# Optimization experiments

Measured on AMD Instinct MI355X. Metric: run time of the kernel, lower is better.

## Reference

```python
import jax, jax.numpy as jnp
import numpy as np

TEMPERATURE = 0.07
TAU_THRESHOLD = 0.5

B, D, K = 32768, 512, 2048


def _l2_normalize(x, axis=-1, eps=1e-12):
    # matches torch F.normalize: x / max(||x||, eps)
    n = jnp.linalg.norm(x, axis=axis, keepdims=True)
    return x / jnp.maximum(n, eps)


def setup_inputs() -> dict:
    key = jax.random.key(0)
    k1, k2, k3, k4 = jax.random.split(key, 4)
    embeddings = jax.random.normal(k1, (B, D), dtype=jnp.float32)
    best_similarity = jax.random.uniform(k2, (B,), dtype=jnp.float32)
    global_prototypes = jax.random.normal(k3, (K, D), dtype=jnp.float32)
    prototype_confidence = jax.random.uniform(k4, (K,), dtype=jnp.float32)
    return {
        "embeddings": embeddings,
        "best_similarity": best_similarity,
        "global_prototypes": global_prototypes,
        "prototype_confidence": prototype_confidence,
    }


def reference(embeddings, best_similarity, global_prototypes, prototype_confidence):
    en = _l2_normalize(embeddings, axis=1)          # [B, D]
    pn = _l2_normalize(global_prototypes, axis=1)   # [K, D]
    sims = jnp.einsum("bd,kd->bk", en, pn)          # [B, K] cosine sims
    best_proto_idx = jnp.argmax(sims, axis=1)       # [B]

    logits = sims / TEMPERATURE
    log_probs = jax.nn.log_softmax(logits, axis=1)  # [B, K]
    probs = jnp.exp(log_probs)
    entropy = -jnp.sum(probs * log_probs, axis=1)   # [B]
    max_entropy = jnp.log(jnp.float32(K))
    entropy_norm = entropy / (max_entropy + 1e-8)
    tau_adaptive = TAU_THRESHOLD - 0.2 * entropy_norm

    # confidence_weighted gating
    batch_conf = prototype_confidence[best_proto_idx]                     # [B]
    sigmoid_gate = jax.nn.sigmoid((best_similarity - tau_adaptive) / TEMPERATURE)
    gate = batch_conf * sigmoid_gate                                      # [B]

    target_protos = pn[best_proto_idx]                                    # [B, D]
    dist = jnp.linalg.norm(en - target_protos, axis=1)                    # [B]
    L_proto = jnp.mean(gate * dist)
    return (L_proto, gate)
```

## Files before the change

### kernel.cpp

```cpp
#include <hip/hip_runtime.h>
#include <math.h>


#define NB 32768
#define ND 512
#define NK 2048
#define TEMPR 0.07f
#define INV_T 14.285714285714286f
#define DX 1.4285714e-4f

typedef unsigned short u16;
typedef unsigned long long u64;
using bf16x8 = __attribute__((ext_vector_type(8))) short;
using u16x8 = __attribute__((ext_vector_type(8))) unsigned short;
using f32x16 = __attribute__((ext_vector_type(16))) float;

__device__ inline u16 bf_hi(float x) {
  unsigned u = __float_as_uint(x);
  u = u + 0x7FFFu + ((u >> 16) & 1u);
  return (u16)(u >> 16);
}
__device__ inline float bf_tof(u16 h) {
  return __uint_as_float(((unsigned)h) << 16);
}
__device__ inline void gload_lds16(const void* g, void* l) {
  __builtin_amdgcn_global_load_lds((const __attribute__((address_space(1))) void*)g,
                                   (__attribute__((address_space(3))) void*)l, 16, 0, 0);
}
#define MF(a, b, c) __builtin_amdgcn_mfma_f32_32x32x16_bf16((a), (b), (c), 0, 0, 0)

#define WAIT_LGKM0 { asm volatile("s_waitcnt lgkmcnt(0)" ::: "memory"); \
                     __builtin_amdgcn_sched_barrier(0); }
#define WAIT_VM10  { asm volatile("s_waitcnt vmcnt(10)" ::: "memory"); \
                     __builtin_amdgcn_sched_barrier(0); }
#define SBAR       { __builtin_amdgcn_s_barrier(); \
                     __builtin_amdgcn_sched_barrier(0); }

__global__ __launch_bounds__(256) void kprep_p(const float* __restrict__ P,
                                               u16* __restrict__ Phi,
                                               u16* __restrict__ Plo,
                                               float* __restrict__ invp,
                                               int* __restrict__ cnt) {
  if (blockIdx.x == 0 && threadIdx.x == 0) *cnt = 0;
  const int lane = threadIdx.x & 63, w = threadIdx.x >> 6;
  const int p = blockIdx.x * 4 + w;
  const float4* pr = (const float4*)(P + (size_t)p * ND);
  float4 a = pr[2 * lane], b = pr[2 * lane + 1];
  float ss = a.x * a.x + a.y * a.y + a.z * a.z + a.w * a.w
           + b.x * b.x + b.y * b.y + b.z * b.z + b.w * b.w;
#pragma unroll
  for (int off = 32; off > 0; off >>= 1) ss += __shfl_xor(ss, off);
  const float inv = 1.0f / fmaxf(sqrtf(ss), 1e-12f);
  if (lane == 0) invp[p] = inv;
  u16x8 h8, l8;
#define PCNV(j, f) { float n_ = (f) * inv; u16 hb_ = bf_hi(n_); \
  h8[j] = hb_; l8[j] = bf_hi(n_ - bf_tof(hb_)); }
  PCNV(0, a.x) PCNV(1, a.y) PCNV(2, a.z) PCNV(3, a.w)
  PCNV(4, b.x) PCNV(5, b.y) PCNV(6, b.z) PCNV(7, b.w)
#undef PCNV
  const int kt = p >> 8, pl = p & 255;
  const size_t idx = ((size_t)((kt * 16 + (lane >> 2)) * 4 + (lane & 3)) * 256 + pl) * 8;
  *(u16x8*)(Phi + idx) = h8;
  *(u16x8*)(Plo + idx) = l8;
}

__global__ __launch_bounds__(256) void kprep_e2(const float* __restrict__ E,
                                                u16* __restrict__ Ehi,
                                                u16* __restrict__ Elo) {
  const int lane = threadIdx.x & 63, w = threadIdx.x >> 6;
  const int row = blockIdx.x * 4 + w;
  const float4* er = (const float4*)(E + (size_t)row * ND);
  float4 a = er[lane], b = er[lane + 64];
  float ss = a.x * a.x + a.y * a.y + a.z * a.z + a.w * a.w
           + b.x * b.x + b.y * b.y + b.z * b.z + b.w * b.w;
#pragma unroll
  for (int off = 32; off > 0; off >>= 1) ss += __shfl_xor(ss, off);
  const float inv = 1.0f / fmaxf(sqrtf(ss), 1e-12f);
  ushort4 h4, l4;
#define PCNV(dst_h, dst_l, f) { float n_ = (f) * inv; u16 hb_ = bf_hi(n_); \
  dst_h = hb_; dst_l = bf_hi(n_ - bf_tof(hb_)); }
  PCNV(h4.x, l4.x, a.x) PCNV(h4.y, l4.y, a.y) PCNV(h4.z, l4.z, a.z) PCNV(h4.w, l4.w, a.w)
  *(ushort4*)(Ehi + (size_t)row * ND + lane * 4) = h4;
  *(ushort4*)(Elo + (size_t)row * ND + lane * 4) = l4;
  PCNV(h4.x, l4.x, b.x) PCNV(h4.y, l4.y, b.y) PCNV(h4.z, l4.z, b.z) PCNV(h4.w, l4.w, b.w)
  *(ushort4*)(Ehi + (size_t)row * ND + (lane + 64) * 4) = h4;
  *(ushort4*)(Elo + (size_t)row * ND + (lane + 64) * 4) = l4;
#undef PCNV
}

#define UPD2(r, vv, pp) { \
  float x_ = fmaf((vv), INV_T, -INV_T); \
  float e_ = __expf(x_); \
  sS[r] += e_; uS[r] = fmaf(x_, e_, uS[r]); \
  bool u1_ = x_ > m1[r]; \
  float lo_ = u1_ ? m1[r] : x_; \
  m2[r] = fmaxf(m2[r], lo_); \
  m1[r] = u1_ ? x_ : m1[r]; \
  ix[r] = u1_ ? (pp) : ix[r]; }

__global__ __launch_bounds__(256, 2) void kmain_v6(
    const float* __restrict__ BS,
    const u16* __restrict__ PhiG, const u16* __restrict__ PloG,
    const u16* __restrict__ EhiG, const u16* __restrict__ EloG,
    const float* __restrict__ CONF,
    float* __restrict__ tau_ws, float* __restrict__ gd, float* __restrict__ gate_out,
    int* __restrict__ cnt, int* __restrict__ flags, u64* __restrict__ pk) {
  __shared__ u16 Ahi[2][2048], Alo[2][2048];
  __shared__ u16 Bhi[2][8192], Blo[2][8192];

  const int t = threadIdx.x;
  const int lane = t & 63;
  const int w = t >> 6, wr = w >> 1, wc = w & 1;
  const int c = lane & 31, h = lane >> 5;
  const int swz = (blockIdx.x & 7) * 64 + (blockIdx.x >> 3);
  const int row0 = swz * 64;

  const u16* EhiA = EhiG + (size_t)(row0 + lane) * ND + w * 8;
  const u16* EloA = EloG + (size_t)(row0 + lane) * ND + w * 8;

  int boff[4];
#pragma unroll
  for (int i = 0; i < 4; ++i) boff[i] = (w * 256 + i * 64 + lane) * 8;

  const int ao0 = ((h)*64 + wr * 32 + c) * 8;
  const int ao1 = ((2 + h) * 64 + wr * 32 + c) * 8;
  const int bo0 = ((h)*256 + wc * 128 + c) * 8;
  const int bo1 = ((2 + h) * 256 + wc * 128 + c) * 8;

  f32x16 acc0, acc1, acc2, acc3;
#pragma unroll
  for (int i = 0; i < 16; ++i) { acc0[i] = 0.f; acc1[i] = 0.f; acc2[i] = 0.f; acc3[i] = 0.f; }
  float sS[16], uS[16], m1[16], m2[16];
  int ix[16];
#pragma unroll
  for (int r = 0; r < 16; ++r) {
    sS[r] = 0.f; uS[r] = 0.f; m1[r] = -3.0e38f; m2[r] = -3.0e38f; ix[r] = 0;
  }

#define SB6(tile_u16, nx) { \
  _Pragma("unroll") \
  for (int i = 0; i < 4; ++i) { \
    gload_lds16(PhiG + (tile_u16) + boff[i], &Bhi[nx][boff[i]]); \
    gload_lds16(PloG + (tile_u16) + boff[i], &Blo[nx][boff[i]]); \
  } }
#define SA6(col, nx) { \
  gload_lds16(EhiA + (col), &Ahi[nx][t * 8]); \
  gload_lds16(EloA + (col), &Alo[nx][t * 8]); }

  SB6(0, 0);
  SA6(0, 0);
  SB6(8192, 1);
  SA6(32, 1);
  WAIT_VM10;
  SBAR;

#pragma unroll 2
  for (int step = 0; step < 128; ++step) {
    const int cur = step & 1;
    const bf16x8 eh0 = *(const bf16x8*)&Ahi[cur][ao0];
    const bf16x8 el0 = *(const bf16x8*)&Alo[cur][ao0];
    const bf16x8 eh1 = *(const bf16x8*)&Ahi[cur][ao1];
    const bf16x8 el1 = *(const bf16x8*)&Alo[cur][ao1];
    const bf16x8 bh00 = *(const bf16x8*)&Bhi[cur][bo0];
    const bf16x8 bh01 = *(const bf16x8*)&Bhi[cur][bo0 + 256];
    const bf16x8 bh02 = *(const bf16x8*)&Bhi[cur][bo0 + 512];
    const bf16x8 bh03 = *(const bf16x8*)&Bhi[cur][bo0 + 768];
    const bf16x8 bl00 = *(const bf16x8*)&Blo[cur][bo0];
    const bf16x8 bl01 = *(const bf16x8*)&Blo[cur][bo0 + 256];
    const bf16x8 bl02 = *(const bf16x8*)&Blo[cur][bo0 + 512];
    const bf16x8 bl03 = *(const bf16x8*)&Blo[cur][bo0 + 768];
    const bf16x8 bh10 = *(const bf16x8*)&Bhi[cur][bo1];
    const bf16x8 bh11 = *(const bf16x8*)&Bhi[cur][bo1 + 256];
    const bf16x8 bh12 = *(const bf16x8*)&Bhi[cur][bo1 + 512];
    const bf16x8 bh13 = *(const bf16x8*)&Bhi[cur][bo1 + 768];
    const bf16x8 bl10 = *(const bf16x8*)&Blo[cur][bo1];
    const bf16x8 bl11 = *(const bf16x8*)&Blo[cur][bo1 + 256];
    const bf16x8 bl12 = *(const bf16x8*)&Blo[cur][bo1 + 512];
    const bf16x8 bl13 = *(const bf16x8*)&Blo[cur][bo1 + 768];

    acc0 = MF(eh0, bh00, acc0); acc1 = MF(eh0, bh01, acc1);
    acc2 = MF(eh0, bh02, acc2); acc3 = MF(eh0, bh03, acc3);
    acc0 = MF(eh0, bl00, acc0); acc1 = MF(eh0, bl01, acc1);
    acc2 = MF(eh0, bl02, acc2); acc3 = MF(eh0, bl03, acc3);
    acc0 = MF(el0, bh00, acc0); acc1 = MF(el0, bh01, acc1);
    acc2 = MF(el0, bh02, acc2); acc3 = MF(el0, bh03, acc3);

    WAIT_LGKM0;
    SBAR;

    const int ns = (step < 126) ? step + 2 : 127;
    SB6(ns * 8192, cur);
    SA6((ns & 15) * 32, cur);

    acc0 = MF(eh1, bh10, acc0); acc1 = MF(eh1, bh11, acc1);
    acc2 = MF(eh1, bh12, acc2); acc3 = MF(eh1, bh13, acc3);
    acc0 = MF(eh1, bl10, acc0); acc1 = MF(eh1, bl11, acc1);
    acc2 = MF(eh1, bl12, acc2); acc3 = MF(eh1, bl13, acc3);
    acc0 = MF(el1, bh10, acc0); acc1 = MF(el1, bh11, acc1);
    acc2 = MF(el1, bh12, acc2); acc3 = MF(el1, bh13, acc3);

    if ((step & 15) == 15) {
      const int pidb = (step >> 4) * 256 + wc * 128 + c;
#pragma unroll
      for (int r = 0; r < 16; ++r) {
        UPD2(r, acc0[r], pidb)
        UPD2(r, acc1[r], pidb + 32)
        UPD2(r, acc2[r], pidb + 64)
        UPD2(r, acc3[r], pidb + 96)
        acc0[r] = 0.f; acc1[r] = 0.f; acc2[r] = 0.f; acc3[r] = 0.f;
      }
    }

    WAIT_VM10;
    SBAR;
  }

  __syncthreads();

#pragma unroll
  for (int off = 1; off < 32; off <<= 1) {
#pragma unroll
    for (int r = 0; r < 16; ++r) {
      float m1o = __shfl_xor(m1[r], off);
      float m2o = __shfl_xor(m2[r], off);
      float so = __shfl_xor(sS[r], off);
      float uo = __shfl_xor(uS[r], off);
      int io = __shfl_xor(ix[r], off);
      sS[r] += so; uS[r] += uo;
      bool up = (m1o > m1[r]) || (m1o == m1[r] && io < ix[r]);
      float losr = (m1o > m1[r]) ? m1[r] : m1o;
      m2[r] = fmaxf(fmaxf(m2[r], m2o), losr);
      m1[r] = fmaxf(m1[r], m1o);
      ix[r] = up ? io : ix[r];
    }
  }

  float* mg = (float*)&Ahi[0][0];
  if (c == 0) {
#pragma unroll
    for (int r = 0; r < 16; ++r) {
      int rowl = (r & 3) + 8 * (r >> 2) + 4 * h;
      int base = ((wr * 2 + wc) * 32 + rowl) * 6;
      mg[base + 0] = m1[r];
      mg[base + 1] = sS[r];
      mg[base + 2] = uS[r];
      mg[base + 3] = __int_as_float(ix[r]);
      mg[base + 4] = m2[r];
    }
  }
  __syncthreads();

  if ((w & 1) == 0 && lane < 32) {
    const int rowl = lane;
    const int b0 = ((wr * 2 + 0) * 32 + rowl) * 6;
    const int b1 = ((wr * 2 + 1) * 32 + rowl) * 6;
    float m1a = mg[b0], s0 = mg[b0 + 1], u0 = mg[b0 + 2];
    int i0 = __float_as_int(mg[b0 + 3]);
    float m2a = mg[b0 + 4];
    float m1b = mg[b1], s1 = mg[b1 + 1], u1 = mg[b1 + 2];
    int i1 = __float_as_int(mg[b1 + 3]);
    float m2b = mg[b1 + 4];

    bool up = (m1b > m1a) || (m1b == m1a && i1 < i0);
    float m = fmaxf(m1a, m1b);
    float m2f = fmaxf(fmaxf(m2a, m2b), fminf(m1a, m1b));
    int idx = up ? i1 : i0;
    bool flg = (m - m2f) < DX;
    float s = s0 + s1, u = u0 + u1;

    float ent = logf(s) - u / s;
    float tau = 0.5f - 0.2f * (ent * (1.0f / (7.6246190071f + 1e-8f)));
    float simmax = fmaf(m, TEMPR, 1.0f);
    float dist = sqrtf(fmaxf(2.0f - 2.0f * simmax, 0.0f));
    int grow = row0 + wr * 32 + rowl;
    float g = CONF[idx] / (1.0f + __expf(-(BS[grow] - tau) * INV_T));
    gate_out[grow] = g;
    gd[grow] = g * dist;
    tau_ws[grow] = tau;
    if (flg) {
      pk[grow] = 0ull;
      int p = atomicAdd(cnt, 1);
      flags[p] = grow;
    }
  }
}

__global__ __launch_bounds__(256) void krescore4(
    const float* __restrict__ E, const float* __restrict__ P,
    const float* __restrict__ invp, const int* __restrict__ cnt,
    const int* __restrict__ flags, u64* __restrict__ pk) {
  const int n = *cnt;
  const int total = n * 16;
  const int t = threadIdx.x;
  const int k = t & 15;
  const int G = t >> 4;

  for (int ch = blockIdx.x; ch < total; ch += gridDim.x) {
    const int j = ch >> 4, q = ch & 15;
    const int row = flags[j];
    float4 e[8];
    float ss = 0.f;
    const float4* er = (const float4*)(E + (size_t)row * ND);
#pragma unroll
    for (int i = 0; i < 8; ++i) {
      e[i] = er[k + 16 * i];
      ss += e[i].x * e[i].x + e[i].y * e[i].y + e[i].z * e[i].z + e[i].w * e[i].w;
    }
#pragma unroll
    for (int o = 1; o < 16; o <<= 1) ss += __shfl_xor(ss, o);
    const float inv = 1.0f / fmaxf(sqrtf(ss), 1e-12f);
#pragma unroll
    for (int i = 0; i < 8; ++i) {
      e[i].x *= inv; e[i].y *= inv; e[i].z *= inv; e[i].w *= inv;
    }

    float best = -3.0e38f;
    int bidx = NK;
#pragma unroll 2
    for (int m = 0; m < 8; ++m) {
      const int p = q * 128 + G + 16 * m;
      const float4* pr = (const float4*)(P + (size_t)p * ND);
      float dot = 0.f;
#pragma unroll
      for (int i = 0; i < 8; ++i) {
        float4 a = pr[k + 16 * i];
        dot = fmaf(a.x, e[i].x, dot); dot = fmaf(a.y, e[i].y, dot);
        dot = fmaf(a.z, e[i].z, dot); dot = fmaf(a.w, e[i].w, dot);
      }
#pragma unroll
      for (int o = 1; o < 16; o <<= 1) dot += __shfl_xor(dot, o);
      float sim = dot * invp[p];
      if (sim > best) { best = sim; bidx = p; }
    }
    if (k == 0) {
      unsigned u = __float_as_uint(best);
      unsigned ord = (u & 0x80000000u) ? ~u : (u | 0x80000000u);
      u64 v = ((u64)ord << 32) | (unsigned)(NK - bidx);
      atomicMax(pk + row, v);
    }
  }
}

__global__ __launch_bounds__(1024) void kreduce2(
    float* __restrict__ gd, const float* __restrict__ BS,
    const float* __restrict__ CONF, const float* __restrict__ tau_ws,
    const int* __restrict__ cnt, const int* __restrict__ flags,
    const u64* __restrict__ pk, float* __restrict__ out0,
    float* __restrict__ gate_out) {
  __shared__ float red[1024];
  const int t = threadIdx.x;

  const int n = *cnt;
  for (int j = t; j < n; j += 1024) {
    const int row = flags[j];
    const u64 v = pk[row];
    const unsigned hi = (unsigned)(v >> 32);
    const int idx = NK - (int)(v & 0xFFFFFFFFu);
    const float sim = (hi & 0x80000000u) ? __uint_as_float(hi & 0x7FFFFFFFu)
                                         : __uint_as_float(~hi);
    const float tau = tau_ws[row];
    const float dist = sqrtf(fmaxf(2.0f - 2.0f * sim, 0.0f));
    const float g = CONF[idx] / (1.0f + __expf(-(BS[row] - tau) * INV_T));
    gate_out[row] = g;
    gd[row] = g * dist;
  }
  __syncthreads();

  float s = 0.f;
  const float4* g4 = (const float4*)gd;
  for (int i = t; i < 8192; i += 1024) {
    float4 v = g4[i];
    s += (v.x + v.y) + (v.z + v.w);
  }
  red[t] = s;
  __syncthreads();
  for (int off = 512; off > 0; off >>= 1) {
    if (t < off) red[t] += red[t + off];
    __syncthreads();
  }
  if (t == 0) out0[0] = red[0] * (1.0f / 32768.0f);
}

extern "C" void kernel_launch(void* const* d_in, const int* in_sizes, int n_in,
                              void* d_out, int out_size, void* d_ws, size_t ws_size,
                              hipStream_t stream) {
  const float* E = (const float*)d_in[0];
  const float* BS = (const float*)d_in[1];
  const float* P = (const float*)d_in[2];
  const float* CONF = (const float*)d_in[3];
  float* out = (float*)d_out;

  char* wsb = (char*)d_ws;
  u16* Phi = (u16*)wsb;
  u16* Plo = (u16*)(wsb + ((size_t)2 << 20));
  u16* Ehi = (u16*)(wsb + ((size_t)4 << 20));
  u16* Elo = (u16*)(wsb + ((size_t)36 << 20));
  char* tail = wsb + ((size_t)68 << 20);
  float* tau_ws = (float*)tail;
  float* gd = (float*)(tail + 131072);
  int* flags = (int*)(tail + 2 * 131072);
  int* cnt = (int*)(tail + 3 * 131072);
  float* invp = (float*)(tail + 3 * 131072 + 4096);
  u64* pk = (u64*)(tail + 3 * 131072 + 4096 + 8192);

  kprep_p<<<512, 256, 0, stream>>>(P, Phi, Plo, invp, cnt);
  kprep_e2<<<8192, 256, 0, stream>>>(E, Ehi, Elo);
  kmain_v6<<<512, 256, 0, stream>>>(BS, Phi, Plo, Ehi, Elo, CONF, tau_ws, gd,
                                    out + 1, cnt, flags, pk);
  krescore4<<<2048, 256, 0, stream>>>(E, P, invp, cnt, flags, pk);
  kreduce2<<<1, 1024, 0, stream>>>(gd, BS, CONF, tau_ws, cnt, flags, pk,
                                   out, out + 1);
}
```

Before: 265.0 us.

## Halve K-tile depth per stage to cut LDS and raise occupancy to three blocks

```diff
diff --git a/kernel.cpp b/kernel.cpp
--- a/kernel.cpp
+++ b/kernel.cpp
@@ -31,7 +31,7 @@
 
 #define WAIT_LGKM0 { asm volatile("s_waitcnt lgkmcnt(0)" ::: "memory"); \
                      __builtin_amdgcn_sched_barrier(0); }
-#define WAIT_VM10  { asm volatile("s_waitcnt vmcnt(10)" ::: "memory"); \
+#define WAIT_VM5   { asm volatile("s_waitcnt vmcnt(5)" ::: "memory"); \
                      __builtin_amdgcn_sched_barrier(0); }
 #define SBAR       { __builtin_amdgcn_s_barrier(); \
                      __builtin_amdgcn_sched_barrier(0); }
@@ -59,7 +59,8 @@
   PCNV(4, b.x) PCNV(5, b.y) PCNV(6, b.z) PCNV(7, b.w)
 #undef PCNV
   const int kt = p >> 8, pl = p & 255;
-  const size_t idx = ((size_t)((kt * 16 + (lane >> 2)) * 4 + (lane & 3)) * 256 + pl) * 8;
+  const size_t idx =
+      ((size_t)((kt * 32 + (lane >> 1)) * 2 + (lane & 1)) * 256 + pl) * 8;
   *(u16x8*)(Phi + idx) = h8;
   *(u16x8*)(Plo + idx) = l8;
 }
@@ -98,15 +99,15 @@
   m1[r] = u1_ ? x_ : m1[r]; \
   ix[r] = u1_ ? (pp) : ix[r]; }
 
-__global__ __launch_bounds__(256, 2) void kmain_v6(
+__global__ __launch_bounds__(256, 3) void kmain_v8(
     const float* __restrict__ BS,
     const u16* __restrict__ PhiG, const u16* __restrict__ PloG,
     const u16* __restrict__ EhiG, const u16* __restrict__ EloG,
     const float* __restrict__ CONF,
     float* __restrict__ tau_ws, float* __restrict__ gd, float* __restrict__ gate_out,
     int* __restrict__ cnt, int* __restrict__ flags, u64* __restrict__ pk) {
-  __shared__ u16 Ahi[2][2048], Alo[2][2048];
-  __shared__ u16 Bhi[2][8192], Blo[2][8192];
+  __shared__ u16 Ahi[2][1024], Alo[2][1024];
+  __shared__ u16 Bhi[2][4096], Blo[2][4096];
 
   const int t = threadIdx.x;
   const int lane = t & 63;
@@ -115,17 +116,16 @@
   const int swz = (blockIdx.x & 7) * 64 + (blockIdx.x >> 3);
   const int row0 = swz * 64;
 
-  const u16* EhiA = EhiG + (size_t)(row0 + lane) * ND + w * 8;
-  const u16* EloA = EloG + (size_t)(row0 + lane) * ND + w * 8;
-
-  int boff[4];
-#pragma unroll
-  for (int i = 0; i < 4; ++i) boff[i] = (w * 256 + i * 64 + lane) * 8;
-
-  const int ao0 = ((h)*64 + wr * 32 + c) * 8;
-  const int ao1 = ((2 + h) * 64 + wr * 32 + c) * 8;
-  const int bo0 = ((h)*256 + wc * 128 + c) * 8;
-  const int bo1 = ((2 + h) * 256 + wc * 128 + c) * 8;
+  const int ag = w & 1;
+  const u16* Asrc = ((w < 2) ? EhiG : EloG) + (size_t)(row0 + lane) * ND + ag * 8;
+  const int aslot = (ag * 64 + lane) * 8;
+
+  int boff[2];
+#pragma unroll
+  for (int i = 0; i < 2; ++i) boff[i] = ((w * 2 + i) * 64 + lane) * 8;
+
+  const int ao0 = (h * 64 + wr * 32 + c) * 8;
+  const int bo0 = (h * 256 + wc * 128 + c) * 8;
 
   f32x16 acc0, acc1, acc2, acc3;
 #pragma unroll
@@ -137,70 +137,54 @@
     sS[r] = 0.f; uS[r] = 0.f; m1[r] = -3.0e38f; m2[r] = -3.0e38f; ix[r] = 0;
   }
 
-#define SB6(tile_u16, nx) { \
+#define SB8(tile_u16, nx) { \
   _Pragma("unroll") \
-  for (int i = 0; i < 4; ++i) { \
+  for (int i = 0; i < 2; ++i) { \
     gload_lds16(PhiG + (tile_u16) + boff[i], &Bhi[nx][boff[i]]); \
     gload_lds16(PloG + (tile_u16) + boff[i], &Blo[nx][boff[i]]); \
   } }
-#define SA6(col, nx) { \
-  gload_lds16(EhiA + (col), &Ahi[nx][t * 8]); \
-  gload_lds16(EloA + (col), &Alo[nx][t * 8]); }
-
-  SB6(0, 0);
-  SA6(0, 0);
-  SB6(8192, 1);
-  SA6(32, 1);
-  WAIT_VM10;
+#define SA8(col, nx) { \
+  if (w < 2) { gload_lds16(Asrc + (col), &Ahi[nx][aslot]); } \
+  else       { gload_lds16(Asrc + (col), &Alo[nx][aslot]); } }
+
+  SB8(0, 0);
+  SA8(0, 0);
+  SB8(4096, 1);
+  SA8(16, 1);
+  WAIT_VM5;
   SBAR;
 
 #pragma unroll 2
-  for (int step = 0; step < 128; ++step) {
+  for (int step = 0; step < 256; ++step) {
     const int cur = step & 1;
-    const bf16x8 eh0 = *(const bf16x8*)&Ahi[cur][ao0];
-    const bf16x8 el0 = *(const bf16x8*)&Alo[cur][ao0];
-    const bf16x8 eh1 = *(const bf16x8*)&Ahi[cur][ao1];
-    const bf16x8 el1 = *(const bf16x8*)&Alo[cur][ao1];
-    const bf16x8 bh00 = *(const bf16x8*)&Bhi[cur][bo0];
-    const bf16x8 bh01 = *(const bf16x8*)&Bhi[cur][bo0 + 256];
-    const bf16x8 bh02 = *(const bf16x8*)&Bhi[cur][bo0 + 512];
-    const bf16x8 bh03 = *(const bf16x8*)&Bhi[cur][bo0 + 768];
-    const bf16x8 bl00 = *(const bf16x8*)&Blo[cur][bo0];
-    const bf16x8 bl01 = *(const bf16x8*)&Blo[cur][bo0 + 256];
-    const bf16x8 bl02 = *(const bf16x8*)&Blo[cur][bo0 + 512];
-    const bf16x8 bl03 = *(const bf16x8*)&Blo[cur][bo0 + 768];
-    const bf16x8 bh10 = *(const bf16x8*)&Bhi[cur][bo1];
-    const bf16x8 bh11 = *(const bf16x8*)&Bhi[cur][bo1 + 256];
-    const bf16x8 bh12 = *(const bf16x8*)&Bhi[cur][bo1 + 512];
-    const bf16x8 bh13 = *(const bf16x8*)&Bhi[cur][bo1 + 768];
-    const bf16x8 bl10 = *(const bf16x8*)&Blo[cur][bo1];
-    const bf16x8 bl11 = *(const bf16x8*)&Blo[cur][bo1 + 256];
-    const bf16x8 bl12 = *(const bf16x8*)&Blo[cur][bo1 + 512];
-    const bf16x8 bl13 = *(const bf16x8*)&Blo[cur][bo1 + 768];
-
-    acc0 = MF(eh0, bh00, acc0); acc1 = MF(eh0, bh01, acc1);
-    acc2 = MF(eh0, bh02, acc2); acc3 = MF(eh0, bh03, acc3);
-    acc0 = MF(eh0, bl00, acc0); acc1 = MF(eh0, bl01, acc1);
-    acc2 = MF(eh0, bl02, acc2); acc3 = MF(eh0, bl03, acc3);
-    acc0 = MF(el0, bh00, acc0); acc1 = MF(el0, bh01, acc1);
-    acc2 = MF(el0, bh02, acc2); acc3 = MF(el0, bh03, acc3);
+    const bf16x8 eh = *(const bf16x8*)&Ahi[cur][ao0];
+    const bf16x8 el = *(const bf16x8*)&Alo[cur][ao0];
+    const bf16x8 bh0 = *(const bf16x8*)&Bhi[cur][bo0];
+    const bf16x8 bh1 = *(const bf16x8*)&Bhi[cur][bo0 + 256];
+    const bf16x8 bh2 = *(const bf16x8*)&Bhi[cur][bo0 + 512];
+    const bf16x8 bh3 = *(const bf16x8*)&Bhi[cur][bo0 + 768];
+    const bf16x8 bl0 = *(const bf16x8*)&Blo[cur][bo0];
+    const bf16x8 bl1 = *(const bf16x8*)&Blo[cur][bo0 + 256];
+    const bf16x8 bl2 = *(const bf16x8*)&Blo[cur][bo0 + 512];
+    const bf16x8 bl3 = *(const bf16x8*)&Blo[cur][bo0 + 768];
+
+    acc0 = MF(eh, bh0, acc0); acc1 = MF(eh, bh1, acc1);
+    acc2 = MF(eh, bh2, acc2); acc3 = MF(eh, bh3, acc3);
 
     WAIT_LGKM0;
     SBAR;
 
-    const int ns = (step < 126) ? step + 2 : 127;
-    SB6(ns * 8192, cur);
-    SA6((ns & 15) * 32, cur);
-
-    acc0 = MF(eh1, bh10, acc0); acc1 = MF(eh1, bh11, acc1);
-    acc2 = MF(eh1, bh12, acc2); acc3 = MF(eh1, bh13, acc3);
-    acc0 = MF(eh1, bl10, acc0); acc1 = MF(eh1, bl11, acc1);
-    acc2 = MF(eh1, bl12, acc2); acc3 = MF(eh1, bl13, acc3);
-    acc0 = MF(el1, bh10, acc0); acc1 = MF(el1, bh11, acc1);
-    acc2 = MF(el1, bh12, acc2); acc3 = MF(el1, bh13, acc3);
-
-    if ((step & 15) == 15) {
-      const int pidb = (step >> 4) * 256 + wc * 128 + c;
+    const int ns = (step < 254) ? step + 2 : 255;
+    SB8(ns * 4096, cur);
+    SA8((ns & 31) * 16, cur);
+
+    acc0 = MF(eh, bl0, acc0); acc1 = MF(eh, bl1, acc1);
+    acc2 = MF(eh, bl2, acc2); acc3 = MF(eh, bl3, acc3);
+    acc0 = MF(el, bh0, acc0); acc1 = MF(el, bh1, acc1);
+    acc2 = MF(el, bh2, acc2); acc3 = MF(el, bh3, acc3);
+
+    if ((step & 31) == 31) {
+      const int pidb = (step >> 5) * 256 + wc * 128 + c;
 #pragma unroll
       for (int r = 0; r < 16; ++r) {
         UPD2(r, acc0[r], pidb)
@@ -211,7 +195,7 @@
       }
     }
 
-    WAIT_VM10;
+    WAIT_VM5;
     SBAR;
   }
 
@@ -405,7 +389,7 @@
 
   kprep_p<<<512, 256, 0, stream>>>(P, Phi, Plo, invp, cnt);
   kprep_e2<<<8192, 256, 0, stream>>>(E, Ehi, Elo);
-  kmain_v6<<<512, 256, 0, stream>>>(BS, Phi, Plo, Ehi, Elo, CONF, tau_ws, gd,
+  kmain_v8<<<512, 256, 0, stream>>>(BS, Phi, Plo, Ehi, Elo, CONF, tau_ws, gd,
                                     out + 1, cnt, flags, pk);
   krescore4<<<2048, 256, 0, stream>>>(E, P, invp, cnt, flags, pk);
   kreduce2<<<1, 1024, 0, stream>>>(gd, BS, CONF, tau_ws, cnt, flags, pk,
```

Result: slower. 959.3 us (+261.9%).
